# Kernel optimization log

Hardware: AMD Instinct MI355X
Metric: run time of the kernel (lower is better)

## Reference

```python
import jax, jax.numpy as jnp
import numpy as np

EMBED_DIM = 1024
N_HEADS = 16
HEAD_DIM = EMBED_DIM // N_HEADS
B, T = 4, 2048


def setup_inputs() -> dict:
    key = jax.random.key(0)
    ks = jax.random.split(key, 5)
    s = 1.0 / np.sqrt(EMBED_DIM)
    return {
        "x": jax.random.normal(ks[0], (B, T, EMBED_DIM), dtype=jnp.float32),
        "w_qkv": jax.random.normal(ks[1], (EMBED_DIM, 3 * EMBED_DIM), dtype=jnp.float32) * s,
        "b_qkv": jnp.zeros((3 * EMBED_DIM,), dtype=jnp.float32),
        "w_out": jax.random.normal(ks[2], (EMBED_DIM, EMBED_DIM), dtype=jnp.float32) * s,
        "b_out": jnp.zeros((EMBED_DIM,), dtype=jnp.float32),
    }


def reference(x, w_qkv, b_qkv, w_out, b_out):
    Bb, Tt, C = x.shape
    qkv = x @ w_qkv + b_qkv                      # (B, T, 3C)
    q, k, v = jnp.split(qkv, 3, axis=-1)
    # (B, H, T, Dh)
    def to_heads(t):
        return t.reshape(Bb, Tt, N_HEADS, HEAD_DIM).transpose(0, 2, 1, 3)
    q, k, v = to_heads(q), to_heads(k), to_heads(v)
    scale = 1.0 / np.sqrt(HEAD_DIM)
    scores = jnp.einsum("bhqd,bhkd->bhqk", q, k) * scale  # (B, H, T, T)
    causal = jnp.tril(jnp.ones((Tt, Tt), dtype=bool))
    scores = jnp.where(causal[None, None], scores, -jnp.inf)
    attn = jax.nn.softmax(scores, axis=-1)
    out = jnp.einsum("bhqk,bhkd->bhqd", attn, v)  # (B, H, T, Dh)
    out = out.transpose(0, 2, 1, 3).reshape(Bb, Tt, C)
    return out @ w_out + b_out
```

## Files before the change

kernel.cpp:

```cpp
#include <hip/hip_runtime.h>

typedef __bf16 bf16;
typedef __bf16 bf16x4 __attribute__((ext_vector_type(4)));
typedef __bf16 bf16x8 __attribute__((ext_vector_type(8)));
typedef float f32x4 __attribute__((ext_vector_type(4)));

#define TSEQ 2048
#define NHEAD 16

#define QSCALE 0.18033688011112042f

#if __has_builtin(__builtin_amdgcn_exp2f)
#define EXP2F(x) __builtin_amdgcn_exp2f(x)
#else
#define EXP2F(x) exp2f(x)
#endif

__device__ __forceinline__ void gload_lds16(const bf16* g, bf16* s) {
  __builtin_amdgcn_global_load_lds(
      (const __attribute__((address_space(1))) void*)g,
      (__attribute__((address_space(3))) void*)s, 16, 0, 0);
}

__global__ __launch_bounds__(256) void prep_kernel(
    const float* __restrict__ x, bf16* __restrict__ xbf,
    const float* __restrict__ w_qkv, bf16* __restrict__ wqkvt,
    const float* __restrict__ w_out, bf16* __restrict__ woutt) {
  __shared__ float tile[32][33];
  const int bid = blockIdx.x;
  const int tid = threadIdx.x;
  if (bid < 4096) {
    size_t i = ((size_t)bid * 256 + tid) * 8;
    float4 v0 = ((const float4*)(x + i))[0];
    float4 v1 = ((const float4*)(x + i))[1];
    bf16x8 o;
    o[0] = (bf16)v0.x; o[1] = (bf16)v0.y; o[2] = (bf16)v0.z; o[3] = (bf16)v0.w;
    o[4] = (bf16)v1.x; o[5] = (bf16)v1.y; o[6] = (bf16)v1.z; o[7] = (bf16)v1.w;
    *(bf16x8*)(xbf + i) = o;
    return;
  }
  const float* in; bf16* out; int K, N, n0, k0;
  if (bid < 7168) {
    int q = bid - 4096;
    in = w_qkv; out = wqkvt; K = 1024; N = 3072;
    n0 = (q % 96) * 32; k0 = (q / 96) * 32;
  } else {
    int q = bid - 7168;
    in = w_out; out = woutt; K = 1024; N = 1024;
    n0 = (q & 31) * 32; k0 = (q >> 5) * 32;
  }
  int tx = tid & 31, ty = tid >> 5;
#pragma unroll
  for (int i = ty; i < 32; i += 8)
    tile[i][tx] = in[(size_t)(k0 + i) * N + n0 + tx];
  __syncthreads();
#pragma unroll
  for (int i = ty; i < 32; i += 8)
    out[(size_t)(n0 + i) * K + k0 + tx] = (bf16)tile[tx][i];
}

template <typename OutT, int BN>
__global__ __launch_bounds__(256, 4) void gemm_bf16_kernel(
    const bf16* __restrict__ A, const bf16* __restrict__ Bt,
    const float* __restrict__ bias, OutT* __restrict__ C,
    int M, int N, int K, int ldc, float scale0, int scale_cols,
    bf16* __restrict__ vp) {
  constexpr int BG = BN / 32;
  constexpr int JN = BN / 32;
  alignas(16) __shared__ bf16 As[128 * 64];
  alignas(16) __shared__ bf16 Bs[BN * 64];
  const int row0 = blockIdx.y * 128, col0 = blockIdx.x * BN;
  const int tid = threadIdx.x;
  const int wave = tid >> 6, lane = tid & 63;
  const int quad = lane >> 4, lm = lane & 15;
  const int wm = (wave >> 1) * 64, wn = (wave & 1) * (BN / 2);

  f32x4 acc[4][JN];
  const f32x4 z4 = {0.0f, 0.0f, 0.0f, 0.0f};
#pragma unroll
  for (int i = 0; i < 4; i++)
#pragma unroll
    for (int j = 0; j < JN; j++) acc[i][j] = z4;

  const int sr0 = tid >> 3;
  const int js = (tid & 7) ^ ((tid >> 4) & 7);
  const bf16* apg = A + (size_t)(row0 + sr0) * K + js * 8;
  const bf16* bpg = Bt + (size_t)(col0 + sr0) * K + js * 8;
  const size_t row32 = (size_t)32 * K;

  const int sw = (lm >> 1) & 7;

  for (int k0 = 0; k0 < K; k0 += 64) {
    __syncthreads();
#pragma unroll
    for (int p = 0; p < 4; p++)
      gload_lds16(apg + p * row32, &As[(p * 256 + tid) * 8]);
#pragma unroll
    for (int p = 0; p < BG; p++)
      gload_lds16(bpg + p * row32, &Bs[(p * 256 + tid) * 8]);
    apg += 64; bpg += 64;
    __syncthreads();

#pragma unroll
    for (int ks = 0; ks < 2; ks++) {
      const int kc = ((ks * 4 + quad) ^ sw) * 8;
      bf16x8 af[4], bfr[JN];
#pragma unroll
      for (int i = 0; i < 4; i++)
        af[i] = *(const bf16x8*)&As[(wm + i * 16 + lm) * 64 + kc];
#pragma unroll
      for (int j = 0; j < JN; j++)
        bfr[j] = *(const bf16x8*)&Bs[(wn + j * 16 + lm) * 64 + kc];
#pragma unroll
      for (int i = 0; i < 4; i++)
#pragma unroll
        for (int j = 0; j < JN; j++)
          acc[i][j] = __builtin_amdgcn_mfma_f32_16x16x32_bf16(af[i], bfr[j], acc[i][j], 0, 0, 0);
    }
  }

#pragma unroll
  for (int j = 0; j < JN; j++) {
    int gc = col0 + wn + j * 16 + lm;
    float bb = bias[gc];
    float sc2 = (gc < scale_cols) ? scale0 : 1.0f;
    if (vp != nullptr && gc >= 2048) {
      int gr0 = row0 + wm + quad * 4;
      int b = gr0 >> 11;
      size_t vrow = (size_t)(b * 1024 + gc - 2048) * TSEQ;
#pragma unroll
      for (int i = 0; i < 4; i++) {
        int t = (gr0 + i * 16) & (TSEQ - 1);
        bf16x4 vk;
#pragma unroll
        for (int rr = 0; rr < 4; rr++) vk[rr] = (bf16)(acc[i][j][rr] + bb);
        *(bf16x4*)(vp + vrow + t) = vk;
      }
    } else {
#pragma unroll
      for (int i = 0; i < 4; i++) {
        int gr = row0 + wm + i * 16 + quad * 4;
#pragma unroll
        for (int rr = 0; rr < 4; rr++) {
          float v = (acc[i][j][rr] + bb) * sc2;
          C[(size_t)(gr + rr) * ldc + gc] = (OutT)v;
        }
      }
    }
  }
}

__global__ __launch_bounds__(256, 4) void flash_attn_kernel(
    const bf16* __restrict__ qk, const bf16* __restrict__ vp,
    bf16* __restrict__ att) {
  alignas(16) __shared__ bf16 Ks[64 * 64];
  alignas(16) __shared__ bf16 Vts[64 * 64];
  alignas(16) __shared__ bf16 Ps[4][32 * 64];

  const int hb = blockIdx.x;
  const int h = hb & 15, b = hb >> 4;
  const int y = blockIdx.y;
  const int g = y >> 2, r = y & 3;
  const int qt = (g == 0) ? (15 - r) : (g == 1) ? r : (g == 2) ? (11 - r) : (4 + r);
  const int q0 = qt * 128;
  const int tid = threadIdx.x;
  const int wave = tid >> 6, lane = tid & 63;
  const int quad = lane >> 4, lm = lane & 15;
  const size_t rowbase = (size_t)b * TSEQ;
  const f32x4 z4 = {0.0f, 0.0f, 0.0f, 0.0f};

  bf16x8 bq[2][2];
#pragma unroll
  for (int nf = 0; nf < 2; nf++)
#pragma unroll
    for (int ks = 0; ks < 2; ks++)
      bq[nf][ks] = *(const bf16x8*)(qk +
          (rowbase + q0 + wave * 32 + nf * 16 + lm) * 2048 + h * 64 + ks * 32 + quad * 8);

  const int strow = tid >> 3;
  const int js = (tid & 7) ^ ((tid >> 4) & 7);
  const bf16* kstg = qk + (rowbase + strow) * 2048 + 1024 + h * 64 + js * 8;
  const bf16* vstg = vp + ((size_t)hb * 64 + strow) * TSEQ + js * 8;
  const size_t krow32 = (size_t)32 * 2048;
  const size_t vrow32 = (size_t)32 * TSEQ;

  const int sw = (lm >> 1) & 7;

  f32x4 oT[4][2];
#pragma unroll
  for (int mf = 0; mf < 4; mf++)
#pragma unroll
    for (int nf = 0; nf < 2; nf++) oT[mf][nf] = z4;
  float lp[2] = {0.0f, 0.0f};

  const int nkt = 2 * qt + 2;
  const int wrow_lo = q0 + wave * 32;
  const int wrow_hi = wrow_lo + 31;

  for (int kt = 0; kt < nkt; kt++) {
    const int k0 = kt * 64;
    __syncthreads();
    gload_lds16(kstg + (size_t)k0 * 2048, &Ks[tid * 8]);
    gload_lds16(kstg + (size_t)k0 * 2048 + krow32, &Ks[(256 + tid) * 8]);
    gload_lds16(vstg + k0, &Vts[tid * 8]);
    gload_lds16(vstg + k0 + vrow32, &Vts[(256 + tid) * 8]);
    __syncthreads();
    if (k0 > wrow_hi) continue;

    f32x4 s[4][2];
#pragma unroll
    for (int mf = 0; mf < 4; mf++)
#pragma unroll
      for (int nf = 0; nf < 2; nf++) s[mf][nf] = z4;
#pragma unroll
    for (int ks = 0; ks < 2; ks++) {
      const int kc = ((ks * 4 + quad) ^ sw) * 8;
      bf16x8 ak[4];
#pragma unroll
      for (int mf = 0; mf < 4; mf++)
        ak[mf] = *(const bf16x8*)&Ks[(mf * 16 + lm) * 64 + kc];
#pragma unroll
      for (int mf = 0; mf < 4; mf++)
#pragma unroll
        for (int nf = 0; nf < 2; nf++)
          s[mf][nf] = __builtin_amdgcn_mfma_f32_16x16x32_bf16(ak[mf], bq[nf][ks], s[mf][nf], 0, 0, 0);
    }

    const bool need_mask = (k0 + 63 > wrow_lo);
#pragma unroll
    for (int nf = 0; nf < 2; nf++) {
      const int qrow = q0 + wave * 32 + nf * 16 + lm;
#pragma unroll
      for (int mf = 0; mf < 4; mf++) {
        bf16x4 pk;
        float psum = 0.0f;
#pragma unroll
        for (int rr = 0; rr < 4; rr++) {
          float pv = EXP2F(s[mf][nf][rr]);
          if (need_mask) {
            int kv = k0 + mf * 16 + quad * 4 + rr;
            pv = (kv > qrow) ? 0.0f : pv;
          }
          psum += pv;
          pk[rr] = (bf16)pv;
        }
        lp[nf] += psum;
        *(bf16x4*)&Ps[wave][(nf * 16 + lm) * 64 +
                            (((mf * 2 + (quad >> 1)) ^ sw) * 8 + (quad & 1) * 4)] = pk;
      }
    }

#pragma unroll
    for (int ks = 0; ks < 2; ks++) {
      const int kc = ((ks * 4 + quad) ^ sw) * 8;
      bf16x8 av[4], bp[2];
#pragma unroll
      for (int mf = 0; mf < 4; mf++)
        av[mf] = *(const bf16x8*)&Vts[(mf * 16 + lm) * 64 + kc];
#pragma unroll
      for (int nf = 0; nf < 2; nf++)
        bp[nf] = *(const bf16x8*)&Ps[wave][(nf * 16 + lm) * 64 + kc];
#pragma unroll
      for (int mf = 0; mf < 4; mf++)
#pragma unroll
        for (int nf = 0; nf < 2; nf++)
          oT[mf][nf] = __builtin_amdgcn_mfma_f32_16x16x32_bf16(av[mf], bp[nf], oT[mf][nf], 0, 0, 0);
    }
  }

  float linv[2];
#pragma unroll
  for (int nf = 0; nf < 2; nf++) {
    float l = lp[nf];
    l += __shfl_xor(l, 16, 64);
    l += __shfl_xor(l, 32, 64);
    linv[nf] = 1.0f / l;
  }

#pragma unroll
  for (int nf = 0; nf < 2; nf++) {
    const size_t grow = rowbase + q0 + wave * 32 + nf * 16 + lm;
#pragma unroll
    for (int mf = 0; mf < 4; mf++) {
      bf16x4 ok;
#pragma unroll
      for (int rr = 0; rr < 4; rr++) ok[rr] = (bf16)(oT[mf][nf][rr] * linv[nf]);
      *(bf16x4*)(att + grow * 1024 + h * 64 + mf * 16 + quad * 4) = ok;
    }
  }
}

extern "C" void kernel_launch(void* const* d_in, const int* in_sizes, int n_in,
                              void* d_out, int out_size, void* d_ws, size_t ws_size,
                              hipStream_t stream) {
  const float* x = (const float*)d_in[0];
  const float* w_qkv = (const float*)d_in[1];
  const float* b_qkv = (const float*)d_in[2];
  const float* w_out = (const float*)d_in[3];
  const float* b_out = (const float*)d_in[4];
  float* out = (float*)d_out;

  char* ws = (char*)d_ws;
  bf16* Xbf   = (bf16*)(ws);
  bf16* ATT   = (bf16*)(ws);
  bf16* Wqkvt = (bf16*)(ws + 16777216);
  bf16* Woutt = (bf16*)(ws + 23068672);
  bf16* QK    = (bf16*)(ws + 25165824);
  bf16* VP    = (bf16*)(ws + 58720256);

  prep_kernel<<<8192, 256, 0, stream>>>(x, Xbf, w_qkv, Wqkvt, w_out, Woutt);
  gemm_bf16_kernel<bf16, 128><<<dim3(24, 64), 256, 0, stream>>>(
      Xbf, Wqkvt, b_qkv, QK, 8192, 3072, 1024, 2048, QSCALE, 1024, VP);
  flash_attn_kernel<<<dim3(64, 16, 1), 256, 0, stream>>>(QK, VP, ATT);
  gemm_bf16_kernel<float, 64><<<dim3(16, 64), 256, 0, stream>>>(
      ATT, Woutt, b_out, out, 8192, 1024, 1024, 1024, 1.0f, 0, nullptr);
}
```

Before: 228.9 us.

## Double-buffer K/V tiles in flash attention and raise MFMA wave priority

Splits the K and V shared-memory tiles into two buffers. The next tile's global-to-LDS loads are issued right after the barrier, so they overlap the current tile's QK^T, softmax and PV work, and one of the two barriers per iteration goes away. The MFMA sections are also wrapped in s_setprio so those waves get scheduling priority. The trade-off is LDS per block rising from 32KB to 48KB, which may cut resident blocks per CU below the launch_bounds target of 4. Correctness also depends on the remaining barrier waiting for the outstanding LDS-direct loads.

```diff
diff --git a/kernel.cpp b/kernel.cpp
--- a/kernel.cpp
+++ b/kernel.cpp
@@ -153,8 +153,8 @@
 __global__ __launch_bounds__(256, 4) void flash_attn_kernel(
     const bf16* __restrict__ qk, const bf16* __restrict__ vp,
     bf16* __restrict__ att) {
-  alignas(16) __shared__ bf16 Ks[64 * 64];
-  alignas(16) __shared__ bf16 Vts[64 * 64];
+  alignas(16) __shared__ bf16 Ks[2][64 * 64];
+  alignas(16) __shared__ bf16 Vts[2][64 * 64];
   alignas(16) __shared__ bf16 Ps[4][32 * 64];
 
   const int hb = blockIdx.x;
@@ -197,34 +197,49 @@
   const int wrow_lo = q0 + wave * 32;
   const int wrow_hi = wrow_lo + 31;
 
+  {
+    gload_lds16(kstg, &Ks[0][tid * 8]);
+    gload_lds16(kstg + krow32, &Ks[0][(256 + tid) * 8]);
+    gload_lds16(vstg, &Vts[0][tid * 8]);
+    gload_lds16(vstg + vrow32, &Vts[0][(256 + tid) * 8]);
+  }
+
   for (int kt = 0; kt < nkt; kt++) {
+    const int cur = kt & 1;
     const int k0 = kt * 64;
     __syncthreads();
-    gload_lds16(kstg + (size_t)k0 * 2048, &Ks[tid * 8]);
-    gload_lds16(kstg + (size_t)k0 * 2048 + krow32, &Ks[(256 + tid) * 8]);
-    gload_lds16(vstg + k0, &Vts[tid * 8]);
-    gload_lds16(vstg + k0 + vrow32, &Vts[(256 + tid) * 8]);
-    __syncthreads();
+    if (kt + 1 < nkt) {
+      const size_t nk0 = (size_t)(k0 + 64);
+      gload_lds16(kstg + nk0 * 2048, &Ks[cur ^ 1][tid * 8]);
+      gload_lds16(kstg + nk0 * 2048 + krow32, &Ks[cur ^ 1][(256 + tid) * 8]);
+      gload_lds16(vstg + nk0, &Vts[cur ^ 1][tid * 8]);
+      gload_lds16(vstg + nk0 + vrow32, &Vts[cur ^ 1][(256 + tid) * 8]);
+    }
     if (k0 > wrow_hi) continue;
 
+    const bf16* kb = &Ks[cur][0];
+    const bf16* vb = &Vts[cur][0];
+
     f32x4 s[4][2];
 #pragma unroll
     for (int mf = 0; mf < 4; mf++)
 #pragma unroll
       for (int nf = 0; nf < 2; nf++) s[mf][nf] = z4;
+    __builtin_amdgcn_s_setprio(1);
 #pragma unroll
     for (int ks = 0; ks < 2; ks++) {
       const int kc = ((ks * 4 + quad) ^ sw) * 8;
       bf16x8 ak[4];
 #pragma unroll
       for (int mf = 0; mf < 4; mf++)
-        ak[mf] = *(const bf16x8*)&Ks[(mf * 16 + lm) * 64 + kc];
+        ak[mf] = *(const bf16x8*)&kb[(mf * 16 + lm) * 64 + kc];
 #pragma unroll
       for (int mf = 0; mf < 4; mf++)
 #pragma unroll
         for (int nf = 0; nf < 2; nf++)
           s[mf][nf] = __builtin_amdgcn_mfma_f32_16x16x32_bf16(ak[mf], bq[nf][ks], s[mf][nf], 0, 0, 0);
     }
+    __builtin_amdgcn_s_setprio(0);
 
     const bool need_mask = (k0 + 63 > wrow_lo);
 #pragma unroll
@@ -250,13 +265,14 @@
       }
     }
 
+    __builtin_amdgcn_s_setprio(1);
 #pragma unroll
     for (int ks = 0; ks < 2; ks++) {
       const int kc = ((ks * 4 + quad) ^ sw) * 8;
       bf16x8 av[4], bp[2];
 #pragma unroll
       for (int mf = 0; mf < 4; mf++)
-        av[mf] = *(const bf16x8*)&Vts[(mf * 16 + lm) * 64 + kc];
+        av[mf] = *(const bf16x8*)&vb[(mf * 16 + lm) * 64 + kc];
 #pragma unroll
       for (int nf = 0; nf < 2; nf++)
         bp[nf] = *(const bf16x8*)&Ps[wave][(nf * 16 + lm) * 64 + kc];
@@ -266,6 +282,7 @@
         for (int nf = 0; nf < 2; nf++)
           oT[mf][nf] = __builtin_amdgcn_mfma_f32_16x16x32_bf16(av[mf], bp[nf], oT[mf][nf], 0, 0, 0);
     }
+    __builtin_amdgcn_s_setprio(0);
   }
 
   float linv[2];
```

Measured after the change: 236.6 us. +3.3%, slower.

## Split long causal query tiles across two blocks and merge partial outputs

Applied to the files above, without the earlier changes.

The attention grid grows from 16 to 24 query-tile slots per head. The heaviest query tiles (8-15) each have their key range split across two blocks. Split blocks write unnormalized fp32 partial outputs and row sums into scratch space, reusing the output buffer and the Wqkv workspace region, and a new merge kernel combines the halves into bf16. This is meant to balance the causal workload across CUs. It costs an extra launch and fp32 scratch traffic, and s_setprio hints are added around the MFMA sections.

```diff
diff --git a/kernel.cpp b/kernel.cpp
--- a/kernel.cpp
+++ b/kernel.cpp
@@ -152,16 +152,22 @@
 
 __global__ __launch_bounds__(256, 4) void flash_attn_kernel(
     const bf16* __restrict__ qk, const bf16* __restrict__ vp,
-    bf16* __restrict__ att) {
+    bf16* __restrict__ att, float* __restrict__ obuf,
+    float* __restrict__ lbuf) {
   alignas(16) __shared__ bf16 Ks[64 * 64];
   alignas(16) __shared__ bf16 Vts[64 * 64];
   alignas(16) __shared__ bf16 Ps[4][32 * 64];
 
+  static const unsigned char QT[24]  = {15, 15,  7, 14, 14, 13, 13,  6, 12, 12, 11, 11,  5, 10, 10,  9,  9,  4,  8,  8,  0,  1,  2,  3};
+  static const unsigned char KLO[24] = { 0, 16,  0,  0, 15,  0, 14,  0,  0, 13,  0, 12,  0,  0, 11,  0, 10,  0,  0,  9,  0,  0,  0,  0};
+  static const unsigned char KHI[24] = {16, 32, 16, 15, 30, 14, 28, 14, 13, 26, 12, 24, 12, 11, 22, 10, 20, 10,  9, 18,  2,  4,  6,  8};
+
   const int hb = blockIdx.x;
   const int h = hb & 15, b = hb >> 4;
   const int y = blockIdx.y;
-  const int g = y >> 2, r = y & 3;
-  const int qt = (g == 0) ? (15 - r) : (g == 1) ? r : (g == 2) ? (11 - r) : (4 + r);
+  const int qt = QT[y];
+  const int klo = KLO[y], khi = KHI[y];
+  const bool is_split = (khi - klo) < (2 * qt + 2);
   const int q0 = qt * 128;
   const int tid = threadIdx.x;
   const int wave = tid >> 6, lane = tid & 63;
@@ -193,11 +199,10 @@
     for (int nf = 0; nf < 2; nf++) oT[mf][nf] = z4;
   float lp[2] = {0.0f, 0.0f};
 
-  const int nkt = 2 * qt + 2;
   const int wrow_lo = q0 + wave * 32;
   const int wrow_hi = wrow_lo + 31;
 
-  for (int kt = 0; kt < nkt; kt++) {
+  for (int kt = klo; kt < khi; kt++) {
     const int k0 = kt * 64;
     __syncthreads();
     gload_lds16(kstg + (size_t)k0 * 2048, &Ks[tid * 8]);
@@ -212,6 +217,7 @@
     for (int mf = 0; mf < 4; mf++)
 #pragma unroll
       for (int nf = 0; nf < 2; nf++) s[mf][nf] = z4;
+    __builtin_amdgcn_s_setprio(1);
 #pragma unroll
     for (int ks = 0; ks < 2; ks++) {
       const int kc = ((ks * 4 + quad) ^ sw) * 8;
@@ -225,6 +231,7 @@
         for (int nf = 0; nf < 2; nf++)
           s[mf][nf] = __builtin_amdgcn_mfma_f32_16x16x32_bf16(ak[mf], bq[nf][ks], s[mf][nf], 0, 0, 0);
     }
+    __builtin_amdgcn_s_setprio(0);
 
     const bool need_mask = (k0 + 63 > wrow_lo);
 #pragma unroll
@@ -250,6 +257,7 @@
       }
     }
 
+    __builtin_amdgcn_s_setprio(1);
 #pragma unroll
     for (int ks = 0; ks < 2; ks++) {
       const int kc = ((ks * 4 + quad) ^ sw) * 8;
@@ -266,28 +274,64 @@
         for (int nf = 0; nf < 2; nf++)
           oT[mf][nf] = __builtin_amdgcn_mfma_f32_16x16x32_bf16(av[mf], bp[nf], oT[mf][nf], 0, 0, 0);
     }
-  }
-
-  float linv[2];
+    __builtin_amdgcn_s_setprio(0);
+  }
+
+  float lsum[2];
 #pragma unroll
   for (int nf = 0; nf < 2; nf++) {
     float l = lp[nf];
     l += __shfl_xor(l, 16, 64);
     l += __shfl_xor(l, 32, 64);
-    linv[nf] = 1.0f / l;
-  }
-
-#pragma unroll
-  for (int nf = 0; nf < 2; nf++) {
-    const size_t grow = rowbase + q0 + wave * 32 + nf * 16 + lm;
-#pragma unroll
-    for (int mf = 0; mf < 4; mf++) {
-      bf16x4 ok;
-#pragma unroll
-      for (int rr = 0; rr < 4; rr++) ok[rr] = (bf16)(oT[mf][nf][rr] * linv[nf]);
-      *(bf16x4*)(att + grow * 1024 + h * 64 + mf * 16 + quad * 4) = ok;
-    }
-  }
+    lsum[nf] = l;
+  }
+
+  if (!is_split) {
+#pragma unroll
+    for (int nf = 0; nf < 2; nf++) {
+      const float linv = 1.0f / lsum[nf];
+      const size_t grow = rowbase + q0 + wave * 32 + nf * 16 + lm;
+#pragma unroll
+      for (int mf = 0; mf < 4; mf++) {
+        bf16x4 ok;
+#pragma unroll
+        for (int rr = 0; rr < 4; rr++) ok[rr] = (bf16)(oT[mf][nf][rr] * linv);
+        *(bf16x4*)(att + grow * 1024 + h * 64 + mf * 16 + quad * 4) = ok;
+      }
+    }
+  } else {
+    const int half = (klo != 0) ? 1 : 0;
+#pragma unroll
+    for (int nf = 0; nf < 2; nf++) {
+      const int qrow = q0 + wave * 32 + nf * 16 + lm;
+      const int ql = qrow - 1024;
+      if (quad == 0) lbuf[(size_t)hb * 2048 + half * 1024 + ql] = lsum[nf];
+      const size_t orow = ((size_t)b * 2048 + (size_t)half * 1024 + ql) * 1024 + h * 64;
+#pragma unroll
+      for (int mf = 0; mf < 4; mf++)
+        *(f32x4*)(obuf + orow + mf * 16 + quad * 4) = oT[mf][nf];
+    }
+  }
+}
+
+__global__ __launch_bounds__(256) void merge_kernel(
+    const float* __restrict__ obuf, const float* __restrict__ lbuf,
+    bf16* __restrict__ att) {
+  const int bq = blockIdx.x;
+  const int b = bq >> 10, ql = bq & 1023;
+  const int c = threadIdx.x * 4;
+  const int h = c >> 6;
+  const size_t base = (size_t)b * 2048 * 1024;
+  const float4 o0 = *(const float4*)(obuf + base + (size_t)ql * 1024 + c);
+  const float4 o1 = *(const float4*)(obuf + base + (size_t)(1024 + ql) * 1024 + c);
+  const size_t lrow = (size_t)(b * 16 + h) * 2048 + ql;
+  const float inv = 1.0f / (lbuf[lrow] + lbuf[lrow + 1024]);
+  bf16x4 o;
+  o[0] = (bf16)((o0.x + o1.x) * inv);
+  o[1] = (bf16)((o0.y + o1.y) * inv);
+  o[2] = (bf16)((o0.z + o1.z) * inv);
+  o[3] = (bf16)((o0.w + o1.w) * inv);
+  *(bf16x4*)(att + ((size_t)b * 2048 + 1024 + ql) * 1024 + c) = o;
 }
 
 extern "C" void kernel_launch(void* const* d_in, const int* in_sizes, int n_in,
@@ -304,6 +348,7 @@
   bf16* Xbf   = (bf16*)(ws);
   bf16* ATT   = (bf16*)(ws);
   bf16* Wqkvt = (bf16*)(ws + 16777216);
+  float* Lbuf = (float*)(ws + 16777216);
   bf16* Woutt = (bf16*)(ws + 23068672);
   bf16* QK    = (bf16*)(ws + 25165824);
   bf16* VP    = (bf16*)(ws + 58720256);
@@ -311,7 +356,8 @@
   prep_kernel<<<8192, 256, 0, stream>>>(x, Xbf, w_qkv, Wqkvt, w_out, Woutt);
   gemm_bf16_kernel<bf16, 128><<<dim3(24, 64), 256, 0, stream>>>(
       Xbf, Wqkvt, b_qkv, QK, 8192, 3072, 1024, 2048, QSCALE, 1024, VP);
-  flash_attn_kernel<<<dim3(64, 16, 1), 256, 0, stream>>>(QK, VP, ATT);
+  flash_attn_kernel<<<dim3(64, 24, 1), 256, 0, stream>>>(QK, VP, ATT, out, Lbuf);
+  merge_kernel<<<4096, 256, 0, stream>>>(out, Lbuf, ATT);
   gemm_bf16_kernel<float, 64><<<dim3(16, 64), 256, 0, stream>>>(
       ATT, Woutt, b_out, out, 8192, 1024, 1024, 1024, 1.0f, 0, nullptr);
 }
```

Result: slower. 236.3 us (+3.2%).

## Load K and V fragments directly from global memory instead of shared LDS staging

Applied to the files above, without the earlier changes.

Drops the block-wide K/V staging in LDS and both __syncthreads per key tile. Each wave now reads its K and V MFMA operands straight from global memory and exits at its own last causal tile instead of idling through the block's extra tiles. It also raises wave priority around the MFMA sections with s_setprio. The cost is that the four waves no longer share K/V loads, so global and L2 traffic rises about fourfold, and load latency is exposed with no prefetch.

```diff
diff --git a/kernel.cpp b/kernel.cpp
--- a/kernel.cpp
+++ b/kernel.cpp
@@ -153,8 +153,6 @@
 __global__ __launch_bounds__(256, 4) void flash_attn_kernel(
     const bf16* __restrict__ qk, const bf16* __restrict__ vp,
     bf16* __restrict__ att) {
-  alignas(16) __shared__ bf16 Ks[64 * 64];
-  alignas(16) __shared__ bf16 Vts[64 * 64];
   alignas(16) __shared__ bf16 Ps[4][32 * 64];
 
   const int hb = blockIdx.x;
@@ -177,12 +175,13 @@
       bq[nf][ks] = *(const bf16x8*)(qk +
           (rowbase + q0 + wave * 32 + nf * 16 + lm) * 2048 + h * 64 + ks * 32 + quad * 8);
 
-  const int strow = tid >> 3;
-  const int js = (tid & 7) ^ ((tid >> 4) & 7);
-  const bf16* kstg = qk + (rowbase + strow) * 2048 + 1024 + h * 64 + js * 8;
-  const bf16* vstg = vp + ((size_t)hb * 64 + strow) * TSEQ + js * 8;
-  const size_t krow32 = (size_t)32 * 2048;
-  const size_t vrow32 = (size_t)32 * TSEQ;
+  const bf16* kp[4];
+  const bf16* vq[4];
+#pragma unroll
+  for (int mf = 0; mf < 4; mf++) {
+    kp[mf] = qk + (rowbase + mf * 16 + lm) * 2048 + 1024 + h * 64 + quad * 8;
+    vq[mf] = vp + ((size_t)hb * 64 + mf * 16 + lm) * TSEQ + quad * 8;
+  }
 
   const int sw = (lm >> 1) & 7;
 
@@ -193,43 +192,36 @@
     for (int nf = 0; nf < 2; nf++) oT[mf][nf] = z4;
   float lp[2] = {0.0f, 0.0f};
 
-  const int nkt = 2 * qt + 2;
   const int wrow_lo = q0 + wave * 32;
-  const int wrow_hi = wrow_lo + 31;
-
-  for (int kt = 0; kt < nkt; kt++) {
+  const int lastkt = (wrow_lo + 31) >> 6;
+
+  for (int kt = 0; kt <= lastkt; kt++) {
     const int k0 = kt * 64;
-    __syncthreads();
-    gload_lds16(kstg + (size_t)k0 * 2048, &Ks[tid * 8]);
-    gload_lds16(kstg + (size_t)k0 * 2048 + krow32, &Ks[(256 + tid) * 8]);
-    gload_lds16(vstg + k0, &Vts[tid * 8]);
-    gload_lds16(vstg + k0 + vrow32, &Vts[(256 + tid) * 8]);
-    __syncthreads();
-    if (k0 > wrow_hi) continue;
 
     f32x4 s[4][2];
 #pragma unroll
     for (int mf = 0; mf < 4; mf++)
 #pragma unroll
       for (int nf = 0; nf < 2; nf++) s[mf][nf] = z4;
+    __builtin_amdgcn_s_setprio(1);
 #pragma unroll
     for (int ks = 0; ks < 2; ks++) {
-      const int kc = ((ks * 4 + quad) ^ sw) * 8;
       bf16x8 ak[4];
 #pragma unroll
       for (int mf = 0; mf < 4; mf++)
-        ak[mf] = *(const bf16x8*)&Ks[(mf * 16 + lm) * 64 + kc];
+        ak[mf] = *(const bf16x8*)(kp[mf] + ks * 32);
 #pragma unroll
       for (int mf = 0; mf < 4; mf++)
 #pragma unroll
         for (int nf = 0; nf < 2; nf++)
           s[mf][nf] = __builtin_amdgcn_mfma_f32_16x16x32_bf16(ak[mf], bq[nf][ks], s[mf][nf], 0, 0, 0);
     }
+    __builtin_amdgcn_s_setprio(0);
 
     const bool need_mask = (k0 + 63 > wrow_lo);
 #pragma unroll
     for (int nf = 0; nf < 2; nf++) {
-      const int qrow = q0 + wave * 32 + nf * 16 + lm;
+      const int qrow = wrow_lo + nf * 16 + lm;
 #pragma unroll
       for (int mf = 0; mf < 4; mf++) {
         bf16x4 pk;
@@ -250,13 +242,14 @@
       }
     }
 
+    __builtin_amdgcn_s_setprio(1);
 #pragma unroll
     for (int ks = 0; ks < 2; ks++) {
       const int kc = ((ks * 4 + quad) ^ sw) * 8;
       bf16x8 av[4], bp[2];
 #pragma unroll
       for (int mf = 0; mf < 4; mf++)
-        av[mf] = *(const bf16x8*)&Vts[(mf * 16 + lm) * 64 + kc];
+        av[mf] = *(const bf16x8*)(vq[mf] + k0 + ks * 32);
 #pragma unroll
       for (int nf = 0; nf < 2; nf++)
         bp[nf] = *(const bf16x8*)&Ps[wave][(nf * 16 + lm) * 64 + kc];
@@ -266,6 +259,10 @@
         for (int nf = 0; nf < 2; nf++)
           oT[mf][nf] = __builtin_amdgcn_mfma_f32_16x16x32_bf16(av[mf], bp[nf], oT[mf][nf], 0, 0, 0);
     }
+    __builtin_amdgcn_s_setprio(0);
+
+#pragma unroll
+    for (int mf = 0; mf < 4; mf++) kp[mf] += (size_t)64 * 2048;
   }
 
   float linv[2];
```

Result: slower. 308.5 us (+34.8%).
